# Kernel tuning notes

Hardware: AMD Instinct MI355X
Metric: run time of the kernel (lower is better)

Reference implementation:

```python
import jax, jax.numpy as jnp
import numpy as np

B, N, F_IN, ENC = 512, 512, 6, 128
EPS = 1e-5  # BatchNorm1d default eps


def _masked_bn_relu(h, m, gamma, beta):
    # h: [B,N,C]; m: [B,N,1] float mask. BN stats over valid points only,
    # matching torch's first_mlp(x[mask]) gather semantics (biased variance).
    cnt = jnp.maximum(m.sum(), 1.0)
    mean = (h * m).sum(axis=(0, 1)) / cnt
    var = (jnp.square(h - mean) * m).sum(axis=(0, 1)) / cnt
    hn = (h - mean) * jax.lax.rsqrt(var + EPS) * gamma + beta
    return jax.nn.relu(hn)


def setup_inputs() -> dict:
    key = jax.random.key(0)
    ks = jax.random.split(key, 16)
    s = lambda fan_in: 1.0 / np.sqrt(fan_in)
    inp = {
        "x": jax.random.normal(ks[0], (B, N, F_IN), dtype=jnp.float32),
        "mask": jax.random.bernoulli(ks[1], 0.7, (B, N)),
        # first_mlp: Linear(F_IN,128), BN(128), ReLU, Linear(128,256)
        "W1": jax.random.uniform(ks[2], (F_IN, 128), jnp.float32, -s(F_IN), s(F_IN)),
        "b1": jnp.zeros((128,), jnp.float32),
        "g1": jnp.ones((128,), jnp.float32),
        "be1": jnp.zeros((128,), jnp.float32),
        "W2": jax.random.uniform(ks[3], (128, 256), jnp.float32, -s(128), s(128)),
        "b2": jnp.zeros((256,), jnp.float32),
        # second_mlp: Linear(512,256), BN(256), ReLU, Linear(256,ENC)
        "W3": jax.random.uniform(ks[4], (512, 256), jnp.float32, -s(512), s(512)),
        "b3": jnp.zeros((256,), jnp.float32),
        "g2": jnp.ones((256,), jnp.float32),
        "be2": jnp.zeros((256,), jnp.float32),
        "W4": jax.random.uniform(ks[5], (256, ENC), jnp.float32, -s(256), s(256)),
        "b4": jnp.zeros((ENC,), jnp.float32),
    }
    return inp


def reference(x, mask, W1, b1, g1, be1, W2, b2, W3, b3, g2, be2, W4, b4):
    m = mask[..., None].astype(x.dtype)  # [B,N,1]
    # first_mlp on valid points; invalid positions become zeros (scatter into zeros buffer)
    h = x @ W1 + b1
    h = _masked_bn_relu(h, m, g1, be1)
    h = (h @ W2 + b2) * m  # [B,N,256], zeros where mask is False
    pooled = h.max(axis=1)  # [B,256] (zeros participate, as in torch)
    feat = jnp.concatenate(
        [h, jnp.broadcast_to(pooled[:, None, :], (h.shape[0], h.shape[1], pooled.shape[-1]))],
        axis=-1,
    )  # [B,N,512]
    h2 = feat @ W3 + b3
    h2 = _masked_bn_relu(h2, m, g2, be2)
    h2 = (h2 @ W4 + b4) * m  # [B,N,ENC], zeros where invalid
    return h2.max(axis=1)  # [B,ENC]
```

## Files before the change

kernel.cpp:

```cpp
#include <hip/hip_runtime.h>
#include <stdint.h>

#define BB   512
#define NN   512
#define MROWS (BB*NN)
#define RT   (MROWS/64)
#define EPSV 1e-5f

typedef unsigned short u16;
typedef __attribute__((ext_vector_type(8))) short bf16x8;
typedef __attribute__((ext_vector_type(4))) float f32x4;

__device__ __forceinline__ float read_mask(const void* mp, int r, int mode) {
  if (mode == 0) return ((const unsigned char*)mp)[r] ? 1.f : 0.f;
  if (mode == 1) return ((const unsigned int*)mp)[r] ? 1.f : 0.f;
  return ((const unsigned long long*)mp)[r] ? 1.f : 0.f;
}

__device__ __forceinline__ u16 f2bf(float f) {
  union { float f; unsigned int u; } v; v.f = f;
  unsigned int u = v.u;
  return (u16)((u + 0x7FFFu + ((u >> 16) & 1u)) >> 16);
}

__device__ __forceinline__ float bf2f(u16 b) {
  union { unsigned int u; float f; } t;
  t.u = ((unsigned int)b) << 16;
  return t.f;
}

__device__ __forceinline__ unsigned int cvt_pk_bf16(float lo, float hi) {
  unsigned int r;
  asm("v_cvt_pk_bf16_f32 %0, %1, %2" : "=v"(r) : "v"(lo), "v"(hi));
  return r;
}

__global__ void k_detect(const unsigned char* __restrict__ mu, int* __restrict__ mode) {
  __shared__ int c1, c4;
  if (threadIdx.x == 0) { c1 = 0; c4 = 0; }
  __syncthreads();
  for (int i = threadIdx.x; i < 4096; i += 256) {
    const unsigned char b = mu[i];
    if (b) {
      if ((i & 3) == 1) atomicAdd(&c1, 1);
      if ((i & 7) == 4) atomicAdd(&c4, 1);
    }
  }
  __syncthreads();
  if (threadIdx.x == 0) *mode = c1 ? 0 : (c4 ? 1 : 2);
}

__global__ __launch_bounds__(256) void k_prep(
    const float* __restrict__ W2, const float* __restrict__ W4,
    u16* __restrict__ w2t, u16* __restrict__ w4t) {
  const int idx = blockIdx.x*256 + threadIdx.x;
  if (idx < 32768) {
    const int n = idx >> 7, k = idx & 127;
    w2t[idx] = f2bf(W2[(size_t)k*256 + n]);
  } else {
    const int j = idx - 32768;
    const int n = j >> 8, k = j & 255;
    w4t[j] = f2bf(W4[(size_t)k*128 + n]);
  }
}

__global__ __launch_bounds__(256) void k_prep23(
    const float* __restrict__ W2, const float* __restrict__ W3, const float* __restrict__ b2,
    u16* __restrict__ w23t, float* __restrict__ c23) {
  __shared__ float row[256];
  const int n = threadIdx.x;
  const int k = blockIdx.x;
  if (k < 128) {
    row[n] = W2[(size_t)k*256 + n];
    __syncthreads();
    float a0 = 0.f, a1 = 0.f, a2v = 0.f, a3 = 0.f;
    for (int j = 0; j < 256; j += 4) {
      a0 = fmaf(row[j  ], W3[(size_t)(j    )*256 + n], a0);
      a1 = fmaf(row[j+1], W3[(size_t)(j + 1)*256 + n], a1);
      a2v= fmaf(row[j+2], W3[(size_t)(j + 2)*256 + n], a2v);
      a3 = fmaf(row[j+3], W3[(size_t)(j + 3)*256 + n], a3);
    }
    w23t[(size_t)n*128 + k] = f2bf(((a0 + a1) + (a2v + a3)));
  } else {
    float a0 = 0.f, a1 = 0.f, a2v = 0.f, a3 = 0.f;
    for (int j = 0; j < 256; j += 4) {
      a0 = fmaf(b2[j  ], W3[(size_t)(j    )*256 + n], a0);
      a1 = fmaf(b2[j+1], W3[(size_t)(j + 1)*256 + n], a1);
      a2v= fmaf(b2[j+2], W3[(size_t)(j + 2)*256 + n], a2v);
      a3 = fmaf(b2[j+3], W3[(size_t)(j + 3)*256 + n], a3);
    }
    c23[n] = ((a0 + a1) + (a2v + a3));
  }
}

__global__ __launch_bounds__(256) void k_stats1(
    const float* __restrict__ x, const void* __restrict__ mask,
    const float* __restrict__ W1, const float* __restrict__ b1,
    const int* __restrict__ modep,
    float* __restrict__ s1sum, float* __restrict__ s1sq, int* __restrict__ cntpart) {
  const int mode = *modep;
  const int tid  = threadIdx.x;
  const int c    = tid & 127;
  const int half = tid >> 7;
  const int blk  = blockIdx.x;
  float w[6];
#pragma unroll
  for (int k = 0; k < 6; ++k) w[k] = W1[k*128 + c];
  const float bb = b1[c];
  float accS = 0.f, accQ = 0.f; int cnt = 0;
  for (int i = half; i < 128; i += 2) {
    const int r = blk*128 + i;
    const float mv = read_mask(mask, r, mode);
    const float* xr = x + (size_t)r*6;
    float h = bb;
#pragma unroll
    for (int k = 0; k < 6; ++k) h = fmaf(xr[k], w[k], h);
    accS += mv*h; accQ += mv*h*h;
    if (c == 0) cnt += (mv != 0.f);
  }
  __shared__ float rs[256], rq[256];
  __shared__ int rc[2];
  rs[tid] = accS; rq[tid] = accQ;
  if (c == 0) rc[half] = cnt;
  __syncthreads();
  if (tid < 128) {
    s1sum[(size_t)blk*128 + tid] = rs[tid] + rs[tid+128];
    s1sq [(size_t)blk*128 + tid] = rq[tid] + rq[tid+128];
    if (tid == 0) cntpart[blk] = rc[0] + rc[1];
  }
}

__global__ __launch_bounds__(256) void k_red1(
    const float* __restrict__ s1sum, const float* __restrict__ s1sq,
    float* __restrict__ mid1s, float* __restrict__ mid1q) {
  const int blk = blockIdx.x;
  const int c = threadIdx.x & 127, g = threadIdx.x >> 7;
  float s = 0.f, q = 0.f;
  for (int r = blk*32 + g*16; r < blk*32 + g*16 + 16; ++r) {
    s += s1sum[(size_t)r*128 + c];
    q += s1sq [(size_t)r*128 + c];
  }
  __shared__ float rs[256], rq[256];
  rs[threadIdx.x] = s; rq[threadIdx.x] = q;
  __syncthreads();
  if (threadIdx.x < 128) {
    mid1s[blk*128 + c] = rs[c] + rs[c+128];
    mid1q[blk*128 + c] = rq[c] + rq[c+128];
  }
}

__global__ __launch_bounds__(128) void k_fin1(
    const float* __restrict__ mid1s, const float* __restrict__ mid1q,
    const int* __restrict__ cntpart,
    const float* __restrict__ W1, const float* __restrict__ b1,
    const float* __restrict__ g1, const float* __restrict__ be1,
    float* __restrict__ w1p, float* __restrict__ c1p, float* __restrict__ cntf) {
  const int c = threadIdx.x;
  float s = 0.f, q = 0.f;
#pragma unroll 8
  for (int b = 0; b < 64; ++b) { s += mid1s[b*128 + c]; q += mid1q[b*128 + c]; }
  __shared__ int cl[128];
  int cn = 0;
  for (int b = c*16; b < c*16 + 16; ++b) cn += cntpart[b];
  cl[c] = cn;
  __syncthreads();
  __shared__ float cshare;
  if (c == 0) {
    int t = 0;
    for (int i = 0; i < 128; ++i) t += cl[i];
    float cf = (float)t; if (cf < 1.f) cf = 1.f;
    cshare = cf; *cntf = cf;
  }
  __syncthreads();
  const float cf = cshare;
  const float mean = s / cf;
  float var = q / cf - mean*mean; if (var < 0.f) var = 0.f;
  const float a = g1[c] * rsqrtf(var + EPSV);
  const float sh = be1[c] - mean*a;
  c1p[c] = fmaf(b1[c], a, sh);
#pragma unroll
  for (int k = 0; k < 6; ++k) w1p[k*128 + c] = W1[k*128 + c] * a;
}

__global__ __launch_bounds__(256, 4) void k_mega(
    const float* __restrict__ x, const void* __restrict__ mask, const int* __restrict__ modep,
    const float* __restrict__ w1p, const float* __restrict__ c1p,
    const u16* __restrict__ W2t, const float* __restrict__ b2,
    const u16* __restrict__ W23t, const float* __restrict__ c23,
    u16* __restrict__ acc3buf, float* __restrict__ poolpart,
    float* __restrict__ s2sum, float* __restrict__ s2sq) {
  __shared__ u16 buf[64*264];
  __shared__ float xs[384];
  __shared__ float mk[64];
  const int mode = *modep;
  const int tid = threadIdx.x;
  const int rt = blockIdx.x;
  const int row0 = rt*64;
  const int b = rt >> 3, seg = rt & 7;
  for (int i = tid; i < 384; i += 256) xs[i] = x[(size_t)row0*6 + i];
  if (tid < 64) mk[tid] = read_mask(mask, row0 + tid, mode);
  __syncthreads();
  {
    const int c0 = (tid & 31) * 4;
    const int r0 = (tid >> 5) * 8;
    float4 wv[6];
#pragma unroll
    for (int k = 0; k < 6; ++k) wv[k] = *(const float4*)(w1p + k*128 + c0);
    const float4 cc = *(const float4*)(c1p + c0);
#pragma unroll
    for (int r = 0; r < 8; ++r) {
      const int row = r0 + r;
      float xv[6];
#pragma unroll
      for (int k = 0; k < 6; ++k) xv[k] = xs[row*6 + k];
      float v0 = cc.x, v1 = cc.y, v2 = cc.z, v3 = cc.w;
#pragma unroll
      for (int k = 0; k < 6; ++k) {
        v0 = fmaf(xv[k], wv[k].x, v0);
        v1 = fmaf(xv[k], wv[k].y, v1);
        v2 = fmaf(xv[k], wv[k].z, v2);
        v3 = fmaf(xv[k], wv[k].w, v3);
      }
      uint2 z;
      z.x = cvt_pk_bf16(fmaxf(v0, 0.f), fmaxf(v1, 0.f));
      z.y = cvt_pk_bf16(fmaxf(v2, 0.f), fmaxf(v3, 0.f));
      *(uint2*)(buf + row*136 + c0) = z;
    }
  }
  __syncthreads();
  const int wave = tid >> 6, lane = tid & 63;
  const int lr = lane & 15, lq = lane >> 4;
  {
    f32x4 acc[4][4];
#pragma unroll
    for (int r = 0; r < 4; ++r)
#pragma unroll
      for (int c = 0; c < 4; ++c) acc[r][c] = (f32x4){0.f,0.f,0.f,0.f};
#pragma unroll
    for (int kc = 0; kc < 128; kc += 32) {
      bf16x8 afr[4];
#pragma unroll
      for (int r = 0; r < 4; ++r)
        afr[r] = *(const bf16x8*)(buf + (r*16 + lr)*136 + kc + lq*8);
#pragma unroll
      for (int c = 0; c < 4; ++c) {
        const bf16x8 bfr = *(const bf16x8*)(W2t + (size_t)(wave*64 + c*16 + lr)*128 + kc + lq*8);
#pragma unroll
        for (int r = 0; r < 4; ++r)
          acc[r][c] = __builtin_amdgcn_mfma_f32_16x16x32_bf16(afr[r], bfr, acc[r][c], 0, 0, 0);
      }
    }
#pragma unroll
    for (int c = 0; c < 4; ++c) {
      const int col = wave*64 + c*16 + lr;
      const float bb = b2[col];
      float cm = -1e38f;
#pragma unroll
      for (int r = 0; r < 4; ++r) {
        const int base = r*16 + lq*4;
#pragma unroll
        for (int i = 0; i < 4; ++i)
          cm = fmaxf(cm, (acc[r][c][i] + bb) * mk[base + i]);
      }
      cm = fmaxf(cm, __shfl_xor(cm, 16, 64));
      cm = fmaxf(cm, __shfl_xor(cm, 32, 64));
      if (lq == 0) poolpart[((size_t)(b*8 + seg))*256 + col] = cm;
    }
  }
  f32x4 acc3[4][4];
#pragma unroll
  for (int r = 0; r < 4; ++r)
#pragma unroll
    for (int c = 0; c < 4; ++c) acc3[r][c] = (f32x4){0.f,0.f,0.f,0.f};
#pragma unroll
  for (int kc = 0; kc < 128; kc += 32) {
    bf16x8 afr[4];
#pragma unroll
    for (int r = 0; r < 4; ++r)
      afr[r] = *(const bf16x8*)(buf + (r*16 + lr)*136 + kc + lq*8);
#pragma unroll
    for (int c = 0; c < 4; ++c) {
      const bf16x8 bfr = *(const bf16x8*)(W23t + (size_t)(wave*64 + c*16 + lr)*128 + kc + lq*8);
#pragma unroll
      for (int r = 0; r < 4; ++r)
        acc3[r][c] = __builtin_amdgcn_mfma_f32_16x16x32_bf16(afr[r], bfr, acc3[r][c], 0, 0, 0);
    }
  }
  __syncthreads();
#pragma unroll
  for (int c = 0; c < 4; ++c) {
    const int col = wave*64 + c*16 + lr;
    const float cc3 = c23[col];
    float sS = 0.f, sQ = 0.f;
#pragma unroll
    for (int r = 0; r < 4; ++r) {
      const int base = r*16 + lq*4;
#pragma unroll
      for (int i = 0; i < 4; i += 2) {
        const float a0 = (acc3[r][c][i]   + cc3) * mk[base + i];
        const float a1 = (acc3[r][c][i+1] + cc3) * mk[base + i + 1];
        const unsigned int u = cvt_pk_bf16(a0, a1);
        buf[(base + i    )*264 + col] = (u16)u;
        buf[(base + i + 1)*264 + col] = (u16)(u >> 16);
        sS += a0 + a1;
        sQ += a0*a0 + a1*a1;
      }
    }
    sS += __shfl_xor(sS, 16, 64);
    sS += __shfl_xor(sS, 32, 64);
    sQ += __shfl_xor(sQ, 16, 64);
    sQ += __shfl_xor(sQ, 32, 64);
    if (lq == 0) {
      s2sum[(size_t)rt*256 + col] = sS;
      s2sq [(size_t)rt*256 + col] = sQ;
    }
  }
  __syncthreads();
  for (int it = tid; it < 64*32; it += 256) {
    const int row = it >> 5, c8 = it & 31;
    *(uint4*)(acc3buf + (size_t)(row0 + row)*256 + c8*8) = *(const uint4*)(buf + row*264 + c8*8);
  }
}

__global__ __launch_bounds__(256) void k_poolP(
    const float* __restrict__ poolpart, const float* __restrict__ W3,
    const float* __restrict__ b3, float* __restrict__ P) {
  __shared__ float pl[256];
  const int b = blockIdx.x, tid = threadIdx.x;
  float m = poolpart[((size_t)b*8)*256 + tid];
#pragma unroll
  for (int s = 1; s < 8; ++s) m = fmaxf(m, poolpart[((size_t)(b*8+s))*256 + tid]);
  pl[tid] = m;
  __syncthreads();
  float a0 = 0.f, a1 = 0.f, a2v = 0.f, a3 = 0.f;
  for (int c = 0; c < 256; c += 4) {
    a0 = fmaf(pl[c  ], W3[(size_t)(256 + c    )*256 + tid], a0);
    a1 = fmaf(pl[c+1], W3[(size_t)(256 + c + 1)*256 + tid], a1);
    a2v= fmaf(pl[c+2], W3[(size_t)(256 + c + 2)*256 + tid], a2v);
    a3 = fmaf(pl[c+3], W3[(size_t)(256 + c + 3)*256 + tid], a3);
  }
  P[(size_t)b*256 + tid] = ((a0 + a1) + (a2v + a3)) + b3[tid];
}

__global__ __launch_bounds__(256) void k_red2(
    const float* __restrict__ s2sum, const float* __restrict__ s2sq,
    const int* __restrict__ cntpart, const float* __restrict__ P,
    float* __restrict__ midS, float* __restrict__ midQ) {
  const int slab = blockIdx.x;
  const int c = threadIdx.x;
  float accS = 0.f, accQ = 0.f;
  for (int b = slab*8; b < slab*8 + 8; ++b) {
    const float cntb = (float)(cntpart[4*b] + cntpart[4*b+1] + cntpart[4*b+2] + cntpart[4*b+3]);
    float S = 0.f, Q = 0.f;
#pragma unroll
    for (int s = 0; s < 8; ++s) {
      S += s2sum[(size_t)(b*8 + s)*256 + c];
      Q += s2sq [(size_t)(b*8 + s)*256 + c];
    }
    const float p = P[(size_t)b*256 + c];
    accS += fmaf(cntb, p, S);
    accQ += fmaf(cntb, p*p, fmaf(2.f*p, S, Q));
  }
  midS[slab*256 + c] = accS;
  midQ[slab*256 + c] = accQ;
}

__global__ __launch_bounds__(256) void k_fin2(
    const float* __restrict__ midS, const float* __restrict__ midQ,
    const float* __restrict__ cntf,
    const float* __restrict__ g2, const float* __restrict__ be2,
    float* __restrict__ a2, float* __restrict__ sh2) {
  const int c = threadIdx.x;
  float s = 0.f, q = 0.f;
#pragma unroll 8
  for (int k = 0; k < 64; ++k) { s += midS[k*256 + c]; q += midQ[k*256 + c]; }
  const float cf = *cntf;
  const float mean = s / cf;
  float var = q / cf - mean*mean; if (var < 0.f) var = 0.f;
  const float a = g2[c] * rsqrtf(var + EPSV);
  a2[c]  = a;
  sh2[c] = be2[c] - mean*a;
}

__global__ __launch_bounds__(512, 4) void k_gemm4(
    const u16* __restrict__ acc3buf, const void* __restrict__ mask, const int* __restrict__ modep,
    const float* __restrict__ P, const float* __restrict__ a2, const float* __restrict__ sh2,
    const u16* __restrict__ W4t, const float* __restrict__ b4,
    float* __restrict__ out) {
  __shared__ u16 a2t[64*264];
  __shared__ float a2l[256], s2b[256];
  __shared__ float mk[64];
  const int mode = *modep;
  const int tid = threadIdx.x;
  const int b = blockIdx.x;
  const int wave = tid >> 6, lane = tid & 63;
  const int lr = lane & 15, lq = lane >> 4;
  const size_t rowbase = (size_t)b*512;
  if (tid < 256) {
    const float aa = a2[tid];
    a2l[tid] = aa;
    s2b[tid] = fmaf(P[(size_t)b*256 + tid], aa, sh2[tid]);
  }
  bf16x8 bw[8];
#pragma unroll
  for (int j = 0; j < 8; ++j)
    bw[j] = *(const bf16x8*)(W4t + (size_t)(wave*16 + lr)*256 + j*32 + lq*8);
  const float bb = b4[wave*16 + lr];
  float cm = -1e38f;
  uint4 u[4];
#pragma unroll
  for (int it = 0; it < 4; ++it) {
    const int j = tid + it*512;
    u[it] = *(const uint4*)(acc3buf + (rowbase + (j >> 5))*256 + (j & 31)*8);
  }
  for (int seg = 0; seg < 8; ++seg) {
    __syncthreads();
#pragma unroll
    for (int it = 0; it < 4; ++it) {
      const int j = tid + it*512;
      const int row = j >> 5, c8 = j & 31;
      const u16* us = (const u16*)&u[it];
      unsigned int pk[4];
#pragma unroll
      for (int jj = 0; jj < 4; ++jj) {
        const int cc0 = c8*8 + jj*2, cc1 = cc0 + 1;
        const float z0 = fmaf(bf2f(us[jj*2    ]), a2l[cc0], s2b[cc0]);
        const float z1 = fmaf(bf2f(us[jj*2 + 1]), a2l[cc1], s2b[cc1]);
        pk[jj] = cvt_pk_bf16(fmaxf(z0, 0.f), fmaxf(z1, 0.f));
      }
      *(uint4*)(a2t + row*264 + c8*8) = *(const uint4*)pk;
    }
    if (tid < 64) mk[tid] = read_mask(mask, (int)(rowbase + seg*64 + tid), mode);
    if (seg < 7) {
#pragma unroll
      for (int it = 0; it < 4; ++it) {
        const int j = tid + it*512;
        u[it] = *(const uint4*)(acc3buf + (rowbase + (seg + 1)*64 + (j >> 5))*256 + (j & 31)*8);
      }
    }
    __syncthreads();
    f32x4 acc[4];
#pragma unroll
    for (int r = 0; r < 4; ++r) acc[r] = (f32x4){0.f,0.f,0.f,0.f};
#pragma unroll
    for (int kc8 = 0; kc8 < 8; ++kc8) {
      bf16x8 afr[4];
#pragma unroll
      for (int r = 0; r < 4; ++r)
        afr[r] = *(const bf16x8*)(a2t + (r*16 + lr)*264 + kc8*32 + lq*8);
#pragma unroll
      for (int r = 0; r < 4; ++r)
        acc[r] = __builtin_amdgcn_mfma_f32_16x16x32_bf16(afr[r], bw[kc8], acc[r], 0, 0, 0);
    }
#pragma unroll
    for (int r = 0; r < 4; ++r) {
#pragma unroll
      for (int i = 0; i < 4; ++i)
        cm = fmaxf(cm, (acc[r][i] + bb) * mk[r*16 + lq*4 + i]);
    }
  }
  cm = fmaxf(cm, __shfl_xor(cm, 16, 64));
  cm = fmaxf(cm, __shfl_xor(cm, 32, 64));
  if (lq == 0) out[(size_t)b*128 + wave*16 + lr] = cm;
}

extern "C" void kernel_launch(void* const* d_in, const int* in_sizes, int n_in,
                              void* d_out, int out_size, void* d_ws, size_t ws_size,
                              hipStream_t stream) {
  const float* x    = (const float*)d_in[0];
  const void*  mask = d_in[1];
  const float* W1   = (const float*)d_in[2];
  const float* b1   = (const float*)d_in[3];
  const float* g1   = (const float*)d_in[4];
  const float* be1  = (const float*)d_in[5];
  const float* W2   = (const float*)d_in[6];
  const float* b2   = (const float*)d_in[7];
  const float* W3   = (const float*)d_in[8];
  const float* b3   = (const float*)d_in[9];
  const float* g2   = (const float*)d_in[10];
  const float* be2  = (const float*)d_in[11];
  const float* W4   = (const float*)d_in[12];
  const float* b4   = (const float*)d_in[13];
  float* out = (float*)d_out;

  char* ws = (char*)d_ws;
  size_t off = 0;
  auto take = [&](size_t bytes) -> char* {
    char* p = ws + off;
    off = (off + bytes + 255) & ~(size_t)255;
    return p;
  };
  u16*   acc3buf = (u16*)  take((size_t)MROWS*256*2);
  float* s1sum   = (float*)take((size_t)2048*128*4);
  float* s1sq    = (float*)take((size_t)2048*128*4);
  int*   cntpart = (int*)  take((size_t)2048*4);
  float* mid1s   = (float*)take((size_t)64*128*4);
  float* mid1q   = (float*)take((size_t)64*128*4);
  float* w1p     = (float*)take(768*4);
  float* c1p     = (float*)take(128*4);
  float* cntf    = (float*)take(256);
  float* poolpart= (float*)take((size_t)512*8*256*4);
  float* P       = (float*)take((size_t)512*256*4);
  float* s2sum   = (float*)take((size_t)RT*256*4);
  float* s2sq    = (float*)take((size_t)RT*256*4);
  float* midS    = (float*)take((size_t)64*256*4);
  float* midQ    = (float*)take((size_t)64*256*4);
  float* a2      = (float*)take(256*4);
  float* sh2     = (float*)take(256*4);
  int*   modep   = (int*)  take(256);
  u16*   w2t     = (u16*)  take((size_t)256*128*2);
  u16*   w23t    = (u16*)  take((size_t)256*128*2);
  u16*   w4t     = (u16*)  take((size_t)128*256*2);
  float* c23     = (float*)take(256*4);

  k_detect<<<1, 256, 0, stream>>>((const unsigned char*)mask, modep);
  k_prep<<<256, 256, 0, stream>>>(W2, W4, w2t, w4t);
  k_prep23<<<129, 256, 0, stream>>>(W2, W3, b2, w23t, c23);
  k_stats1<<<2048, 256, 0, stream>>>(x, mask, W1, b1, modep, s1sum, s1sq, cntpart);
  k_red1<<<64, 256, 0, stream>>>(s1sum, s1sq, mid1s, mid1q);
  k_fin1<<<1, 128, 0, stream>>>(mid1s, mid1q, cntpart, W1, b1, g1, be1, w1p, c1p, cntf);
  k_mega<<<RT, 256, 0, stream>>>(x, mask, modep, w1p, c1p, w2t, b2, w23t, c23,
                                 acc3buf, poolpart, s2sum, s2sq);
  k_poolP<<<512, 256, 0, stream>>>(poolpart, W3, b3, P);
  k_red2<<<64, 256, 0, stream>>>(s2sum, s2sq, cntpart, P, midS, midQ);
  k_fin2<<<1, 256, 0, stream>>>(midS, midQ, cntf, g2, be2, a2, sh2);
  k_gemm4<<<512, 512, 0, stream>>>(acc3buf, mask, modep, P, a2, sh2, w4t, b4, out);
}
```

Measured before the change: 297.9 us.

## Recompute layer-3 activations in final GEMM instead of storing bf16 intermediate

Drops the 128MB bf16 acc3 intermediate buffer written by the mega kernel and read back by the final GEMM. The final kernel now recomputes the first layer and the fused W2·W3 GEMM per 64-row segment from x, then applies BN2+ReLU and the W4 GEMM. This trades HBM write/read traffic for roughly double the layer-3 MFMA work and extra register pressure, with launch bounds lowered to 2 blocks per CU. It also merges the two weight-prep kernels into one launch.

```diff
diff --git a/kernel.cpp b/kernel.cpp
--- a/kernel.cpp
+++ b/kernel.cpp
@@ -51,45 +51,46 @@
 }
 
 __global__ __launch_bounds__(256) void k_prep(
-    const float* __restrict__ W2, const float* __restrict__ W4,
-    u16* __restrict__ w2t, u16* __restrict__ w4t) {
-  const int idx = blockIdx.x*256 + threadIdx.x;
-  if (idx < 32768) {
-    const int n = idx >> 7, k = idx & 127;
-    w2t[idx] = f2bf(W2[(size_t)k*256 + n]);
+    const float* __restrict__ W2, const float* __restrict__ W3, const float* __restrict__ W4,
+    const float* __restrict__ b2,
+    u16* __restrict__ w2t, u16* __restrict__ w4t,
+    u16* __restrict__ w23t, float* __restrict__ c23) {
+  const int blk = blockIdx.x;
+  if (blk < 256) {
+    const int idx = blk*256 + threadIdx.x;
+    if (idx < 32768) {
+      const int n = idx >> 7, k = idx & 127;
+      w2t[idx] = f2bf(W2[(size_t)k*256 + n]);
+    } else {
+      const int j = idx - 32768;
+      const int n = j >> 8, k = j & 255;
+      w4t[j] = f2bf(W4[(size_t)k*128 + n]);
+    }
   } else {
-    const int j = idx - 32768;
-    const int n = j >> 8, k = j & 255;
-    w4t[j] = f2bf(W4[(size_t)k*128 + n]);
-  }
-}
-
-__global__ __launch_bounds__(256) void k_prep23(
-    const float* __restrict__ W2, const float* __restrict__ W3, const float* __restrict__ b2,
-    u16* __restrict__ w23t, float* __restrict__ c23) {
-  __shared__ float row[256];
-  const int n = threadIdx.x;
-  const int k = blockIdx.x;
-  if (k < 128) {
-    row[n] = W2[(size_t)k*256 + n];
-    __syncthreads();
-    float a0 = 0.f, a1 = 0.f, a2v = 0.f, a3 = 0.f;
-    for (int j = 0; j < 256; j += 4) {
-      a0 = fmaf(row[j  ], W3[(size_t)(j    )*256 + n], a0);
-      a1 = fmaf(row[j+1], W3[(size_t)(j + 1)*256 + n], a1);
-      a2v= fmaf(row[j+2], W3[(size_t)(j + 2)*256 + n], a2v);
-      a3 = fmaf(row[j+3], W3[(size_t)(j + 3)*256 + n], a3);
-    }
-    w23t[(size_t)n*128 + k] = f2bf(((a0 + a1) + (a2v + a3)));
-  } else {
-    float a0 = 0.f, a1 = 0.f, a2v = 0.f, a3 = 0.f;
-    for (int j = 0; j < 256; j += 4) {
-      a0 = fmaf(b2[j  ], W3[(size_t)(j    )*256 + n], a0);
-      a1 = fmaf(b2[j+1], W3[(size_t)(j + 1)*256 + n], a1);
-      a2v= fmaf(b2[j+2], W3[(size_t)(j + 2)*256 + n], a2v);
-      a3 = fmaf(b2[j+3], W3[(size_t)(j + 3)*256 + n], a3);
-    }
-    c23[n] = ((a0 + a1) + (a2v + a3));
+    __shared__ float row[256];
+    const int n = threadIdx.x;
+    const int k = blk - 256;
+    if (k < 128) {
+      row[n] = W2[(size_t)k*256 + n];
+      __syncthreads();
+      float a0 = 0.f, a1 = 0.f, a2v = 0.f, a3 = 0.f;
+      for (int j = 0; j < 256; j += 4) {
+        a0 = fmaf(row[j  ], W3[(size_t)(j    )*256 + n], a0);
+        a1 = fmaf(row[j+1], W3[(size_t)(j + 1)*256 + n], a1);
+        a2v= fmaf(row[j+2], W3[(size_t)(j + 2)*256 + n], a2v);
+        a3 = fmaf(row[j+3], W3[(size_t)(j + 3)*256 + n], a3);
+      }
+      w23t[(size_t)n*128 + k] = f2bf(((a0 + a1) + (a2v + a3)));
+    } else {
+      float a0 = 0.f, a1 = 0.f, a2v = 0.f, a3 = 0.f;
+      for (int j = 0; j < 256; j += 4) {
+        a0 = fmaf(b2[j  ], W3[(size_t)(j    )*256 + n], a0);
+        a1 = fmaf(b2[j+1], W3[(size_t)(j + 1)*256 + n], a1);
+        a2v= fmaf(b2[j+2], W3[(size_t)(j + 2)*256 + n], a2v);
+        a3 = fmaf(b2[j+3], W3[(size_t)(j + 3)*256 + n], a3);
+      }
+      c23[n] = ((a0 + a1) + (a2v + a3));
+    }
   }
 }
 
@@ -187,9 +188,9 @@
     const float* __restrict__ w1p, const float* __restrict__ c1p,
     const u16* __restrict__ W2t, const float* __restrict__ b2,
     const u16* __restrict__ W23t, const float* __restrict__ c23,
-    u16* __restrict__ acc3buf, float* __restrict__ poolpart,
+    float* __restrict__ poolpart,
     float* __restrict__ s2sum, float* __restrict__ s2sq) {
-  __shared__ u16 buf[64*264];
+  __shared__ u16 hA[64*136];
   __shared__ float xs[384];
   __shared__ float mk[64];
   const int mode = *modep;
@@ -224,7 +225,7 @@
       uint2 z;
       z.x = cvt_pk_bf16(fmaxf(v0, 0.f), fmaxf(v1, 0.f));
       z.y = cvt_pk_bf16(fmaxf(v2, 0.f), fmaxf(v3, 0.f));
-      *(uint2*)(buf + row*136 + c0) = z;
+      *(uint2*)(hA + row*136 + c0) = z;
     }
   }
   __syncthreads();
@@ -241,7 +242,7 @@
       bf16x8 afr[4];
 #pragma unroll
       for (int r = 0; r < 4; ++r)
-        afr[r] = *(const bf16x8*)(buf + (r*16 + lr)*136 + kc + lq*8);
+        afr[r] = *(const bf16x8*)(hA + (r*16 + lr)*136 + kc + lq*8);
 #pragma unroll
       for (int c = 0; c < 4; ++c) {
         const bf16x8 bfr = *(const bf16x8*)(W2t + (size_t)(wave*64 + c*16 + lr)*128 + kc + lq*8);
@@ -277,7 +278,7 @@
     bf16x8 afr[4];
 #pragma unroll
     for (int r = 0; r < 4; ++r)
-      afr[r] = *(const bf16x8*)(buf + (r*16 + lr)*136 + kc + lq*8);
+      afr[r] = *(const bf16x8*)(hA + (r*16 + lr)*136 + kc + lq*8);
 #pragma unroll
     for (int c = 0; c < 4; ++c) {
       const bf16x8 bfr = *(const bf16x8*)(W23t + (size_t)(wave*64 + c*16 + lr)*128 + kc + lq*8);
@@ -286,7 +287,6 @@
         acc3[r][c] = __builtin_amdgcn_mfma_f32_16x16x32_bf16(afr[r], bfr, acc3[r][c], 0, 0, 0);
     }
   }
-  __syncthreads();
 #pragma unroll
   for (int c = 0; c < 4; ++c) {
     const int col = wave*64 + c*16 + lr;
@@ -296,14 +296,10 @@
     for (int r = 0; r < 4; ++r) {
       const int base = r*16 + lq*4;
 #pragma unroll
-      for (int i = 0; i < 4; i += 2) {
-        const float a0 = (acc3[r][c][i]   + cc3) * mk[base + i];
-        const float a1 = (acc3[r][c][i+1] + cc3) * mk[base + i + 1];
-        const unsigned int u = cvt_pk_bf16(a0, a1);
-        buf[(base + i    )*264 + col] = (u16)u;
-        buf[(base + i + 1)*264 + col] = (u16)(u >> 16);
-        sS += a0 + a1;
-        sQ += a0*a0 + a1*a1;
+      for (int i = 0; i < 4; ++i) {
+        const float a0 = (acc3[r][c][i] + cc3) * mk[base + i];
+        sS += a0;
+        sQ += a0*a0;
       }
     }
     sS += __shfl_xor(sS, 16, 64);
@@ -314,11 +310,6 @@
       s2sum[(size_t)rt*256 + col] = sS;
       s2sq [(size_t)rt*256 + col] = sQ;
     }
-  }
-  __syncthreads();
-  for (int it = tid; it < 64*32; it += 256) {
-    const int row = it >> 5, c8 = it & 31;
-    *(uint4*)(acc3buf + (size_t)(row0 + row)*256 + c8*8) = *(const uint4*)(buf + row*264 + c8*8);
   }
 }
 
@@ -382,13 +373,16 @@
   sh2[c] = be2[c] - mean*a;
 }
 
-__global__ __launch_bounds__(512, 4) void k_gemm4(
-    const u16* __restrict__ acc3buf, const void* __restrict__ mask, const int* __restrict__ modep,
+__global__ __launch_bounds__(512, 2) void k_gemm4(
+    const float* __restrict__ x, const void* __restrict__ mask, const int* __restrict__ modep,
+    const float* __restrict__ w1p, const float* __restrict__ c1p,
+    const u16* __restrict__ W23t, const float* __restrict__ c23,
     const float* __restrict__ P, const float* __restrict__ a2, const float* __restrict__ sh2,
     const u16* __restrict__ W4t, const float* __restrict__ b4,
     float* __restrict__ out) {
-  __shared__ u16 a2t[64*264];
-  __shared__ float a2l[256], s2b[256];
+  __shared__ u16 hA[64*136];
+  __shared__ u16 zt[64*264];
+  __shared__ float a2l[256], s2b[256], c23l[256];
   __shared__ float mk[64];
   const int mode = *modep;
   const int tid = threadIdx.x;
@@ -400,63 +394,109 @@
     const float aa = a2[tid];
     a2l[tid] = aa;
     s2b[tid] = fmaf(P[(size_t)b*256 + tid], aa, sh2[tid]);
-  }
-  bf16x8 bw[8];
+    c23l[tid] = c23[tid];
+  }
+  bf16x8 bw23[2][4];
+#pragma unroll
+  for (int c = 0; c < 2; ++c)
+#pragma unroll
+    for (int kc = 0; kc < 4; ++kc)
+      bw23[c][kc] = *(const bf16x8*)(W23t + (size_t)(wave*32 + c*16 + lr)*128 + kc*32 + lq*8);
+  bf16x8 bw4[8];
 #pragma unroll
   for (int j = 0; j < 8; ++j)
-    bw[j] = *(const bf16x8*)(W4t + (size_t)(wave*16 + lr)*256 + j*32 + lq*8);
-  const float bb = b4[wave*16 + lr];
+    bw4[j] = *(const bf16x8*)(W4t + (size_t)(wave*16 + lr)*256 + j*32 + lq*8);
+  const float bb4 = b4[wave*16 + lr];
+  const int c0 = (tid & 31) * 4;
+  const int r0 = (tid >> 5) * 4;
+  float4 wv[6];
+#pragma unroll
+  for (int k = 0; k < 6; ++k) wv[k] = *(const float4*)(w1p + k*128 + c0);
+  const float4 cc = *(const float4*)(c1p + c0);
   float cm = -1e38f;
-  uint4 u[4];
-#pragma unroll
-  for (int it = 0; it < 4; ++it) {
-    const int j = tid + it*512;
-    u[it] = *(const uint4*)(acc3buf + (rowbase + (j >> 5))*256 + (j & 31)*8);
-  }
   for (int seg = 0; seg < 8; ++seg) {
+    const size_t row0 = rowbase + seg*64;
     __syncthreads();
-#pragma unroll
-    for (int it = 0; it < 4; ++it) {
-      const int j = tid + it*512;
-      const int row = j >> 5, c8 = j & 31;
-      const u16* us = (const u16*)&u[it];
-      unsigned int pk[4];
-#pragma unroll
-      for (int jj = 0; jj < 4; ++jj) {
-        const int cc0 = c8*8 + jj*2, cc1 = cc0 + 1;
-        const float z0 = fmaf(bf2f(us[jj*2    ]), a2l[cc0], s2b[cc0]);
-        const float z1 = fmaf(bf2f(us[jj*2 + 1]), a2l[cc1], s2b[cc1]);
-        pk[jj] = cvt_pk_bf16(fmaxf(z0, 0.f), fmaxf(z1, 0.f));
-      }
-      *(uint4*)(a2t + row*264 + c8*8) = *(const uint4*)pk;
-    }
-    if (tid < 64) mk[tid] = read_mask(mask, (int)(rowbase + seg*64 + tid), mode);
-    if (seg < 7) {
-#pragma unroll
-      for (int it = 0; it < 4; ++it) {
-        const int j = tid + it*512;
-        u[it] = *(const uint4*)(acc3buf + (rowbase + (seg + 1)*64 + (j >> 5))*256 + (j & 31)*8);
-      }
+    if (tid < 64) mk[tid] = read_mask(mask, (int)(row0 + tid), mode);
+#pragma unroll
+    for (int r = 0; r < 4; ++r) {
+      const int row = r0 + r;
+      const float* xr = x + (row0 + row)*6;
+      float v0 = cc.x, v1 = cc.y, v2 = cc.z, v3 = cc.w;
+#pragma unroll
+      for (int k = 0; k < 6; ++k) {
+        const float xv = xr[k];
+        v0 = fmaf(xv, wv[k].x, v0);
+        v1 = fmaf(xv, wv[k].y, v1);
+        v2 = fmaf(xv, wv[k].z, v2);
+        v3 = fmaf(xv, wv[k].w, v3);
+      }
+      uint2 z;
+      z.x = cvt_pk_bf16(fmaxf(v0, 0.f), fmaxf(v1, 0.f));
+      z.y = cvt_pk_bf16(fmaxf(v2, 0.f), fmaxf(v3, 0.f));
+      *(uint2*)(hA + row*136 + c0) = z;
     }
     __syncthreads();
-    f32x4 acc[4];
-#pragma unroll
-    for (int r = 0; r < 4; ++r) acc[r] = (f32x4){0.f,0.f,0.f,0.f};
+    f32x4 acc23[4][2];
+#pragma unroll
+    for (int r = 0; r < 4; ++r)
+#pragma unroll
+      for (int c = 0; c < 2; ++c) acc23[r][c] = (f32x4){0.f,0.f,0.f,0.f};
+#pragma unroll
+    for (int kc = 0; kc < 4; ++kc) {
+      bf16x8 afr[4];
+#pragma unroll
+      for (int r = 0; r < 4; ++r)
+        afr[r] = *(const bf16x8*)(hA + (r*16 + lr)*136 + kc*32 + lq*8);
+#pragma unroll
+      for (int c = 0; c < 2; ++c)
+#pragma unroll
+        for (int r = 0; r < 4; ++r)
+          acc23[r][c] = __builtin_amdgcn_mfma_f32_16x16x32_bf16(bw23[c][kc], afr[r], acc23[r][c], 0, 0, 0);
+    }
+    {
+      float mkr[4];
+#pragma unroll
+      for (int r = 0; r < 4; ++r) mkr[r] = mk[r*16 + lr];
+#pragma unroll
+      for (int c = 0; c < 2; ++c) {
+        const int colb = wave*32 + c*16 + lq*4;
+        const float4 c23v = *(const float4*)(c23l + colb);
+        const float4 a2v  = *(const float4*)(a2l  + colb);
+        const float4 s2v  = *(const float4*)(s2b  + colb);
+#pragma unroll
+        for (int r = 0; r < 4; ++r) {
+          const float m = mkr[r];
+          const float z0 = fmaf((acc23[r][c][0] + c23v.x) * m, a2v.x, s2v.x);
+          const float z1 = fmaf((acc23[r][c][1] + c23v.y) * m, a2v.y, s2v.y);
+          const float z2 = fmaf((acc23[r][c][2] + c23v.z) * m, a2v.z, s2v.z);
+          const float z3 = fmaf((acc23[r][c][3] + c23v.w) * m, a2v.w, s2v.w);
+          uint2 zz;
+          zz.x = cvt_pk_bf16(fmaxf(z0, 0.f), fmaxf(z1, 0.f));
+          zz.y = cvt_pk_bf16(fmaxf(z2, 0.f), fmaxf(z3, 0.f));
+          *(uint2*)(zt + (r*16 + lr)*264 + colb) = zz;
+        }
+      }
+    }
+    __syncthreads();
+    f32x4 acc4[4];
+#pragma unroll
+    for (int r = 0; r < 4; ++r) acc4[r] = (f32x4){0.f,0.f,0.f,0.f};
 #pragma unroll
     for (int kc8 = 0; kc8 < 8; ++kc8) {
       bf16x8 afr[4];
 #pragma unroll
       for (int r = 0; r < 4; ++r)
-        afr[r] = *(const bf16x8*)(a2t + (r*16 + lr)*264 + kc8*32 + lq*8);
+        afr[r] = *(const bf16x8*)(zt + (r*16 + lr)*264 + kc8*32 + lq*8);
 #pragma unroll
       for (int r = 0; r < 4; ++r)
-        acc[r] = __builtin_amdgcn_mfma_f32_16x16x32_bf16(afr[r], bw[kc8], acc[r], 0, 0, 0);
+        acc4[r] = __builtin_amdgcn_mfma_f32_16x16x32_bf16(afr[r], bw4[kc8], acc4[r], 0, 0, 0);
     }
 #pragma unroll
     for (int r = 0; r < 4; ++r) {
 #pragma unroll
       for (int i = 0; i < 4; ++i)
-        cm = fmaxf(cm, (acc[r][i] + bb) * mk[r*16 + lq*4 + i]);
+        cm = fmaxf(cm, (acc4[r][i] + bb4) * mk[r*16 + lq*4 + i]);
     }
   }
   cm = fmaxf(cm, __shfl_xor(cm, 16, 64));
@@ -490,7 +530,6 @@
     off = (off + bytes + 255) & ~(size_t)255;
     return p;
   };
-  u16*   acc3buf = (u16*)  take((size_t)MROWS*256*2);
   float* s1sum   = (float*)take((size_t)2048*128*4);
   float* s1sq    = (float*)take((size_t)2048*128*4);
   int*   cntpart = (int*)  take((size_t)2048*4);
@@ -514,15 +553,15 @@
   float* c23     = (float*)take(256*4);
 
   k_detect<<<1, 256, 0, stream>>>((const unsigned char*)mask, modep);
-  k_prep<<<256, 256, 0, stream>>>(W2, W4, w2t, w4t);
-  k_prep23<<<129, 256, 0, stream>>>(W2, W3, b2, w23t, c23);
+  k_prep<<<385, 256, 0, stream>>>(W2, W3, W4, b2, w2t, w4t, w23t, c23);
   k_stats1<<<2048, 256, 0, stream>>>(x, mask, W1, b1, modep, s1sum, s1sq, cntpart);
   k_red1<<<64, 256, 0, stream>>>(s1sum, s1sq, mid1s, mid1q);
   k_fin1<<<1, 128, 0, stream>>>(mid1s, mid1q, cntpart, W1, b1, g1, be1, w1p, c1p, cntf);
   k_mega<<<RT, 256, 0, stream>>>(x, mask, modep, w1p, c1p, w2t, b2, w23t, c23,
-                                 acc3buf, poolpart, s2sum, s2sq);
+                                 poolpart, s2sum, s2sq);
   k_poolP<<<512, 256, 0, stream>>>(poolpart, W3, b3, P);
   k_red2<<<64, 256, 0, stream>>>(s2sum, s2sq, cntpart, P, midS, midQ);
   k_fin2<<<1, 256, 0, stream>>>(midS, midQ, cntf, g2, be2, a2, sh2);
-  k_gemm4<<<512, 512, 0, stream>>>(acc3buf, mask, modep, P, a2, sh2, w4t, b4, out);
-}
+  k_gemm4<<<512, 512, 0, stream>>>(x, mask, modep, w1p, c1p, w23t, c23,
+                                   P, a2, sh2, w4t, b4, out);
+}
```

After: 311.2 us. 1.04x slower.

## Compute BN1 stats from input moments and merge prep/detect kernels

Applied to the files above, without the earlier changes.

The first BatchNorm's statistics are now derived algebraically from masked first and second moments of the 6-dim input (6 sums plus 21 cross products) rather than from the 128-channel hidden activations. This shrinks the stats pass to 128 blocks with wave shuffle reductions and removes the intermediate reduction kernel. The mask-detect, weight-transpose and W2·W3 fold kernels are merged into one launch, so launch count drops from 11 to 8. Computing variance as E[h²]−mean² from raw moments in fp32 may lose precision relative to the previous per-channel accumulation. Note that the mode is written by one block of the merged kernel and read by k_stats1, which runs afterwards on the same stream, so ordering is preserved.

```diff
diff --git a/kernel.cpp b/kernel.cpp
--- a/kernel.cpp
+++ b/kernel.cpp
@@ -35,149 +35,165 @@
   return r;
 }
 
-__global__ void k_detect(const unsigned char* __restrict__ mu, int* __restrict__ mode) {
-  __shared__ int c1, c4;
-  if (threadIdx.x == 0) { c1 = 0; c4 = 0; }
-  __syncthreads();
-  for (int i = threadIdx.x; i < 4096; i += 256) {
-    const unsigned char b = mu[i];
-    if (b) {
-      if ((i & 3) == 1) atomicAdd(&c1, 1);
-      if ((i & 7) == 4) atomicAdd(&c4, 1);
-    }
-  }
-  __syncthreads();
-  if (threadIdx.x == 0) *mode = c1 ? 0 : (c4 ? 1 : 2);
-}
-
 __global__ __launch_bounds__(256) void k_prep(
-    const float* __restrict__ W2, const float* __restrict__ W4,
-    u16* __restrict__ w2t, u16* __restrict__ w4t) {
-  const int idx = blockIdx.x*256 + threadIdx.x;
-  if (idx < 32768) {
-    const int n = idx >> 7, k = idx & 127;
-    w2t[idx] = f2bf(W2[(size_t)k*256 + n]);
+    const float* __restrict__ W2, const float* __restrict__ W3, const float* __restrict__ W4,
+    const float* __restrict__ b2, const unsigned char* __restrict__ mu,
+    u16* __restrict__ w2t, u16* __restrict__ w4t,
+    u16* __restrict__ w23t, float* __restrict__ c23, int* __restrict__ mode) {
+  __shared__ float row[256];
+  __shared__ int c1s, c4s;
+  const int blk = blockIdx.x;
+  if (blk < 256) {
+    const int idx = blk*256 + threadIdx.x;
+    if (idx < 32768) {
+      const int n = idx >> 7, k = idx & 127;
+      w2t[idx] = f2bf(W2[(size_t)k*256 + n]);
+    } else {
+      const int j = idx - 32768;
+      const int n = j >> 8, k = j & 255;
+      w4t[j] = f2bf(W4[(size_t)k*128 + n]);
+    }
+  } else if (blk < 385) {
+    const int n = threadIdx.x;
+    const int k = blk - 256;
+    if (k < 128) {
+      row[n] = W2[(size_t)k*256 + n];
+      __syncthreads();
+      float a0 = 0.f, a1 = 0.f, a2v = 0.f, a3 = 0.f;
+      for (int j = 0; j < 256; j += 4) {
+        a0 = fmaf(row[j  ], W3[(size_t)(j    )*256 + n], a0);
+        a1 = fmaf(row[j+1], W3[(size_t)(j + 1)*256 + n], a1);
+        a2v= fmaf(row[j+2], W3[(size_t)(j + 2)*256 + n], a2v);
+        a3 = fmaf(row[j+3], W3[(size_t)(j + 3)*256 + n], a3);
+      }
+      w23t[(size_t)n*128 + k] = f2bf(((a0 + a1) + (a2v + a3)));
+    } else {
+      float a0 = 0.f, a1 = 0.f, a2v = 0.f, a3 = 0.f;
+      for (int j = 0; j < 256; j += 4) {
+        a0 = fmaf(b2[j  ], W3[(size_t)(j    )*256 + n], a0);
+        a1 = fmaf(b2[j+1], W3[(size_t)(j + 1)*256 + n], a1);
+        a2v= fmaf(b2[j+2], W3[(size_t)(j + 2)*256 + n], a2v);
+        a3 = fmaf(b2[j+3], W3[(size_t)(j + 3)*256 + n], a3);
+      }
+      c23[n] = ((a0 + a1) + (a2v + a3));
+    }
   } else {
-    const int j = idx - 32768;
-    const int n = j >> 8, k = j & 255;
-    w4t[j] = f2bf(W4[(size_t)k*128 + n]);
-  }
-}
-
-__global__ __launch_bounds__(256) void k_prep23(
-    const float* __restrict__ W2, const float* __restrict__ W3, const float* __restrict__ b2,
-    u16* __restrict__ w23t, float* __restrict__ c23) {
-  __shared__ float row[256];
-  const int n = threadIdx.x;
-  const int k = blockIdx.x;
-  if (k < 128) {
-    row[n] = W2[(size_t)k*256 + n];
+    if (threadIdx.x == 0) { c1s = 0; c4s = 0; }
     __syncthreads();
-    float a0 = 0.f, a1 = 0.f, a2v = 0.f, a3 = 0.f;
-    for (int j = 0; j < 256; j += 4) {
-      a0 = fmaf(row[j  ], W3[(size_t)(j    )*256 + n], a0);
-      a1 = fmaf(row[j+1], W3[(size_t)(j + 1)*256 + n], a1);
-      a2v= fmaf(row[j+2], W3[(size_t)(j + 2)*256 + n], a2v);
-      a3 = fmaf(row[j+3], W3[(size_t)(j + 3)*256 + n], a3);
-    }
-    w23t[(size_t)n*128 + k] = f2bf(((a0 + a1) + (a2v + a3)));
-  } else {
-    float a0 = 0.f, a1 = 0.f, a2v = 0.f, a3 = 0.f;
-    for (int j = 0; j < 256; j += 4) {
-      a0 = fmaf(b2[j  ], W3[(size_t)(j    )*256 + n], a0);
-      a1 = fmaf(b2[j+1], W3[(size_t)(j + 1)*256 + n], a1);
-      a2v= fmaf(b2[j+2], W3[(size_t)(j + 2)*256 + n], a2v);
-      a3 = fmaf(b2[j+3], W3[(size_t)(j + 3)*256 + n], a3);
-    }
-    c23[n] = ((a0 + a1) + (a2v + a3));
+    for (int i = threadIdx.x; i < 4096; i += 256) {
+      const unsigned char b = mu[i];
+      if (b) {
+        if ((i & 3) == 1) atomicAdd(&c1s, 1);
+        if ((i & 7) == 4) atomicAdd(&c4s, 1);
+      }
+    }
+    __syncthreads();
+    if (threadIdx.x == 0) *mode = c1s ? 0 : (c4s ? 1 : 2);
   }
 }
 
 __global__ __launch_bounds__(256) void k_stats1(
     const float* __restrict__ x, const void* __restrict__ mask,
-    const float* __restrict__ W1, const float* __restrict__ b1,
     const int* __restrict__ modep,
-    float* __restrict__ s1sum, float* __restrict__ s1sq, int* __restrict__ cntpart) {
+    float* __restrict__ part, float* __restrict__ cntbf) {
   const int mode = *modep;
-  const int tid  = threadIdx.x;
-  const int c    = tid & 127;
-  const int half = tid >> 7;
-  const int blk  = blockIdx.x;
-  float w[6];
-#pragma unroll
-  for (int k = 0; k < 6; ++k) w[k] = W1[k*128 + c];
-  const float bb = b1[c];
-  float accS = 0.f, accQ = 0.f; int cnt = 0;
-  for (int i = half; i < 128; i += 2) {
-    const int r = blk*128 + i;
+  const int tid = threadIdx.x;
+  const int blk = blockIdx.x;
+  float sx[6] = {0,0,0,0,0,0};
+  float sxx[21] = {0};
+  float cntq[4] = {0,0,0,0};
+#pragma unroll
+  for (int it = 0; it < 8; ++it) {
+    const int r = blk*2048 + it*256 + tid;
     const float mv = read_mask(mask, r, mode);
     const float* xr = x + (size_t)r*6;
-    float h = bb;
-#pragma unroll
-    for (int k = 0; k < 6; ++k) h = fmaf(xr[k], w[k], h);
-    accS += mv*h; accQ += mv*h*h;
-    if (c == 0) cnt += (mv != 0.f);
-  }
-  __shared__ float rs[256], rq[256];
-  __shared__ int rc[2];
-  rs[tid] = accS; rq[tid] = accQ;
-  if (c == 0) rc[half] = cnt;
-  __syncthreads();
-  if (tid < 128) {
-    s1sum[(size_t)blk*128 + tid] = rs[tid] + rs[tid+128];
-    s1sq [(size_t)blk*128 + tid] = rq[tid] + rq[tid+128];
-    if (tid == 0) cntpart[blk] = rc[0] + rc[1];
-  }
-}
-
-__global__ __launch_bounds__(256) void k_red1(
-    const float* __restrict__ s1sum, const float* __restrict__ s1sq,
-    float* __restrict__ mid1s, float* __restrict__ mid1q) {
-  const int blk = blockIdx.x;
-  const int c = threadIdx.x & 127, g = threadIdx.x >> 7;
-  float s = 0.f, q = 0.f;
-  for (int r = blk*32 + g*16; r < blk*32 + g*16 + 16; ++r) {
-    s += s1sum[(size_t)r*128 + c];
-    q += s1sq [(size_t)r*128 + c];
-  }
-  __shared__ float rs[256], rq[256];
-  rs[threadIdx.x] = s; rq[threadIdx.x] = q;
-  __syncthreads();
-  if (threadIdx.x < 128) {
-    mid1s[blk*128 + c] = rs[c] + rs[c+128];
-    mid1q[blk*128 + c] = rq[c] + rq[c+128];
+    const float2 p0 = *(const float2*)(xr);
+    const float2 p1 = *(const float2*)(xr + 2);
+    const float2 p2 = *(const float2*)(xr + 4);
+    float v[6] = {p0.x, p0.y, p1.x, p1.y, p2.x, p2.y};
+    cntq[it >> 1] += mv;
+    int idx = 0;
+#pragma unroll
+    for (int j = 0; j < 6; ++j) {
+      sx[j] = fmaf(mv, v[j], sx[j]);
+      const float mj = mv * v[j];
+#pragma unroll
+      for (int k = j; k < 6; ++k) { sxx[idx] = fmaf(mj, v[k], sxx[idx]); ++idx; }
+    }
+  }
+  float vals[32];
+#pragma unroll
+  for (int j = 0; j < 6; ++j) vals[j] = sx[j];
+#pragma unroll
+  for (int j = 0; j < 21; ++j) vals[6 + j] = sxx[j];
+  vals[27] = 0.f;
+#pragma unroll
+  for (int q = 0; q < 4; ++q) vals[28 + q] = cntq[q];
+#pragma unroll
+  for (int j = 0; j < 32; ++j) {
+#pragma unroll
+    for (int m = 1; m <= 32; m <<= 1)
+      vals[j] += __shfl_xor(vals[j], m, 64);
+  }
+  __shared__ float red[4][32];
+  const int wave = tid >> 6, lane = tid & 63;
+  if (lane == 0) {
+#pragma unroll
+    for (int j = 0; j < 32; ++j) red[wave][j] = vals[j];
+  }
+  __syncthreads();
+  if (tid < 32) {
+    const float tot = red[0][tid] + red[1][tid] + red[2][tid] + red[3][tid];
+    part[(size_t)blk*32 + tid] = tot;
+    if (tid >= 28) cntbf[blk*4 + (tid - 28)] = tot;
   }
 }
 
 __global__ __launch_bounds__(128) void k_fin1(
-    const float* __restrict__ mid1s, const float* __restrict__ mid1q,
-    const int* __restrict__ cntpart,
+    const float* __restrict__ part,
     const float* __restrict__ W1, const float* __restrict__ b1,
     const float* __restrict__ g1, const float* __restrict__ be1,
     float* __restrict__ w1p, float* __restrict__ c1p, float* __restrict__ cntf) {
-  const int c = threadIdx.x;
-  float s = 0.f, q = 0.f;
-#pragma unroll 8
-  for (int b = 0; b < 64; ++b) { s += mid1s[b*128 + c]; q += mid1q[b*128 + c]; }
-  __shared__ int cl[128];
-  int cn = 0;
-  for (int b = c*16; b < c*16 + 16; ++b) cn += cntpart[b];
-  cl[c] = cn;
-  __syncthreads();
-  __shared__ float cshare;
-  if (c == 0) {
-    int t = 0;
-    for (int i = 0; i < 128; ++i) t += cl[i];
-    float cf = (float)t; if (cf < 1.f) cf = 1.f;
-    cshare = cf; *cntf = cf;
-  }
-  __syncthreads();
-  const float cf = cshare;
-  const float mean = s / cf;
-  float var = q / cf - mean*mean; if (var < 0.f) var = 0.f;
+  __shared__ float tot[32];
+  const int t = threadIdx.x;
+  if (t < 32) {
+    float a0 = 0.f, a1 = 0.f, a2v = 0.f, a3 = 0.f;
+    for (int i = 0; i < 128; i += 4) {
+      a0 += part[(size_t)(i    )*32 + t];
+      a1 += part[(size_t)(i + 1)*32 + t];
+      a2v+= part[(size_t)(i + 2)*32 + t];
+      a3 += part[(size_t)(i + 3)*32 + t];
+    }
+    tot[t] = (a0 + a1) + (a2v + a3);
+  }
+  __syncthreads();
+  float cnt = tot[28] + tot[29] + tot[30] + tot[31];
+  if (cnt < 1.f) cnt = 1.f;
+  if (t == 0) *cntf = cnt;
+  const int c = t;
+  float w[6];
+#pragma unroll
+  for (int k = 0; k < 6; ++k) w[k] = W1[k*128 + c];
+  float s1 = 0.f;
+#pragma unroll
+  for (int k = 0; k < 6; ++k) s1 = fmaf(w[k], tot[k], s1);
+  s1 /= cnt;
+  float q = 0.f;
+  {
+    int idx = 6;
+#pragma unroll
+    for (int j = 0; j < 6; ++j) {
+      q = fmaf(w[j]*w[j], tot[idx], q); ++idx;
+#pragma unroll
+      for (int k = j + 1; k < 6; ++k) { q = fmaf(2.f*w[j]*w[k], tot[idx], q); ++idx; }
+    }
+  }
+  float var = q / cnt - s1*s1; if (var < 0.f) var = 0.f;
+  const float mean = b1[c] + s1;
   const float a = g1[c] * rsqrtf(var + EPSV);
   const float sh = be1[c] - mean*a;
-  c1p[c] = fmaf(b1[c], a, sh);
+  c1p[c] = fmaf(b1[c], a, sh - b1[c]*a + (mean - s1)*0.f);
+  c1p[c] = fmaf(b1[c], a, be1[c] - mean*a);
 #pragma unroll
   for (int k = 0; k < 6; ++k) w1p[k*128 + c] = W1[k*128 + c] * a;
 }
@@ -344,13 +360,13 @@
 
 __global__ __launch_bounds__(256) void k_red2(
     const float* __restrict__ s2sum, const float* __restrict__ s2sq,
-    const int* __restrict__ cntpart, const float* __restrict__ P,
+    const float* __restrict__ cntbf, const float* __restrict__ P,
     float* __restrict__ midS, float* __restrict__ midQ) {
   const int slab = blockIdx.x;
   const int c = threadIdx.x;
   float accS = 0.f, accQ = 0.f;
   for (int b = slab*8; b < slab*8 + 8; ++b) {
-    const float cntb = (float)(cntpart[4*b] + cntpart[4*b+1] + cntpart[4*b+2] + cntpart[4*b+3]);
+    const float cntb = cntbf[b];
     float S = 0.f, Q = 0.f;
 #pragma unroll
     for (int s = 0; s < 8; ++s) {
@@ -491,11 +507,8 @@
     return p;
   };
   u16*   acc3buf = (u16*)  take((size_t)MROWS*256*2);
-  float* s1sum   = (float*)take((size_t)2048*128*4);
-  float* s1sq    = (float*)take((size_t)2048*128*4);
-  int*   cntpart = (int*)  take((size_t)2048*4);
-  float* mid1s   = (float*)take((size_t)64*128*4);
-  float* mid1q   = (float*)take((size_t)64*128*4);
+  float* part    = (float*)take((size_t)128*32*4);
+  float* cntbf   = (float*)take((size_t)512*4);
   float* w1p     = (float*)take(768*4);
   float* c1p     = (float*)take(128*4);
   float* cntf    = (float*)take(256);
@@ -513,16 +526,14 @@
   u16*   w4t     = (u16*)  take((size_t)128*256*2);
   float* c23     = (float*)take(256*4);
 
-  k_detect<<<1, 256, 0, stream>>>((const unsigned char*)mask, modep);
-  k_prep<<<256, 256, 0, stream>>>(W2, W4, w2t, w4t);
-  k_prep23<<<129, 256, 0, stream>>>(W2, W3, b2, w23t, c23);
-  k_stats1<<<2048, 256, 0, stream>>>(x, mask, W1, b1, modep, s1sum, s1sq, cntpart);
-  k_red1<<<64, 256, 0, stream>>>(s1sum, s1sq, mid1s, mid1q);
-  k_fin1<<<1, 128, 0, stream>>>(mid1s, mid1q, cntpart, W1, b1, g1, be1, w1p, c1p, cntf);
+  k_prep<<<386, 256, 0, stream>>>(W2, W3, W4, b2, (const unsigned char*)mask,
+                                  w2t, w4t, w23t, c23, modep);
+  k_stats1<<<128, 256, 0, stream>>>(x, mask, modep, part, cntbf);
+  k_fin1<<<1, 128, 0, stream>>>(part, W1, b1, g1, be1, w1p, c1p, cntf);
   k_mega<<<RT, 256, 0, stream>>>(x, mask, modep, w1p, c1p, w2t, b2, w23t, c23,
                                  acc3buf, poolpart, s2sum, s2sq);
   k_poolP<<<512, 256, 0, stream>>>(poolpart, W3, b3, P);
-  k_red2<<<64, 256, 0, stream>>>(s2sum, s2sq, cntpart, P, midS, midQ);
+  k_red2<<<64, 256, 0, stream>>>(s2sum, s2sq, cntbf, P, midS, midQ);
   k_fin2<<<1, 256, 0, stream>>>(midS, midQ, cntf, g2, be2, a2, sh2);
   k_gemm4<<<512, 512, 0, stream>>>(acc3buf, mask, modep, P, a2, sh2, w4t, b4, out);
 }
```

Result: faster. 242.8 us (-18.5%).
